# Kernel tuning notes

Measured on AMD Instinct MI355X. Metric: run time of the kernel, lower is better.

Reference implementation:

```python
import jax, jax.numpy as jnp
import numpy as np

N, D, INNER, HIDDEN, CLASSES = 2048, 64, 32, 2048, 10
P = D * (D - 1) // 2  # 2016 pairwise units


def setup_inputs() -> dict:
    key = jax.random.key(0)
    k = jax.random.split(key, 7)
    x = jax.random.normal(k[0], (N, D), dtype=jnp.float32)
    # pairwise Linear(2, inner): stacked weights [P, 2, INNER]
    Wu = jax.random.normal(k[1], (P, 2, INNER), dtype=jnp.float32) * (1.0 / np.sqrt(2.0))
    bu = jax.random.normal(k[2], (P, INNER), dtype=jnp.float32) * 0.01
    Wv = jax.random.normal(k[3], (P * INNER, HIDDEN), dtype=jnp.float32) * (1.0 / np.sqrt(P * INNER))
    bv = jax.random.normal(k[4], (HIDDEN,), dtype=jnp.float32) * 0.01
    Wo = jax.random.normal(k[5], (HIDDEN, CLASSES), dtype=jnp.float32) * (1.0 / np.sqrt(HIDDEN))
    bo = jax.random.normal(k[6], (CLASSES,), dtype=jnp.float32) * 0.01
    return {"x": x, "Wu": Wu, "bu": bu, "Wv": Wv, "bv": bv, "Wo": Wo, "bo": bo}


def reference(x, Wu, bu, Wv, bv, Wo, bo):
    d = x.shape[1]
    ii, jj = np.triu_indices(d, k=1)  # static pair indices, P pairs
    # gather all pairwise 2-vectors in one shot: [N, P, 2]
    pairs = jnp.stack([x[:, ii], x[:, jj]], axis=-1)
    # fused batched tiny matmuls + ReLU: [N, P, INNER]
    u = jax.nn.relu(jnp.einsum('npt,pti->npi', pairs, Wu) + bu)
    u_concat = u.reshape(u.shape[0], -1)  # [N, P*INNER]
    v = jax.nn.relu(u_concat @ Wv + bv)   # [N, HIDDEN]
    return v @ Wo + bo                    # [N, CLASSES]
```

## Files before the change

kernel.cpp:

```cpp
#include <hip/hip_runtime.h>
#include <stdint.h>
#include <stddef.h>

#define N_ 2048
#define D_ 64
#define INNER_ 32
#define HIDDEN_ 2048
#define CLASSES_ 10
#define P_ 2016
#define K_ (P_ * INNER_)
#define SPLITK 4
#define KCHUNK (K_ / SPLITK)
#define BM 128
#define BN 128
#define BK 32
#define TBM 256
#define TBN 256
#define TBK 16
#define NBUF 4

typedef __bf16 bf16x8 __attribute__((ext_vector_type(8)));
typedef __bf16 bf16x4 __attribute__((ext_vector_type(4)));
typedef float f32x16 __attribute__((ext_vector_type(16)));
typedef float f32x4v __attribute__((ext_vector_type(4)));
typedef float f32x2v __attribute__((ext_vector_type(2)));
typedef __attribute__((address_space(1))) void gvoid_t;
typedef __attribute__((address_space(3))) void lvoid_t;

__global__ __launch_bounds__(256) void k_u(const float* __restrict__ x,
                                           const float* __restrict__ Wu,
                                           const float* __restrict__ bu,
                                           __bf16* __restrict__ u) {
  const int t = threadIdx.x;
  const int n0 = blockIdx.y * 4;
  __shared__ float xs[4][D_];
  __shared__ int iis[32], jjs[32];
  xs[t >> 6][t & 63] = x[(size_t)(n0 + (t >> 6)) * D_ + (t & 63)];
  if (t < 32) {
    const int p = blockIdx.x * 32 + t;
    int ii = (int)floorf((127.0f - sqrtf(16129.0f - 8.0f * (float)p)) * 0.5f);
    int off = ii * 63 - (ii * (ii - 1)) / 2;
    while (p >= off + (63 - ii)) { off += 63 - ii; ++ii; }
    while (p < off)              { --ii; off -= 63 - ii; }
    iis[t] = ii;
    jjs[t] = (p - off) + ii + 1;
  }
  __syncthreads();
  const int k0 = blockIdx.x * 1024 + t * 4;
  const int pl = t >> 3;
  const int i0 = (t & 7) * 4;
  const int p  = blockIdx.x * 32 + pl;
  const float4 w0 = *(const float4*)(Wu + (size_t)p * 64 + i0);
  const float4 w1 = *(const float4*)(Wu + (size_t)p * 64 + 32 + i0);
  const float4 bb = *(const float4*)(bu + (size_t)p * 32 + i0);
  const int ii = iis[pl], jj = jjs[pl];
#pragma unroll
  for (int nn = 0; nn < 4; ++nn) {
    const float xi = xs[nn][ii], xj = xs[nn][jj];
    bf16x4 r;
    r[0] = (__bf16)fmaxf(fmaf(xi, w0.x, fmaf(xj, w1.x, bb.x)), 0.0f);
    r[1] = (__bf16)fmaxf(fmaf(xi, w0.y, fmaf(xj, w1.y, bb.y)), 0.0f);
    r[2] = (__bf16)fmaxf(fmaf(xi, w0.z, fmaf(xj, w1.z, bb.z)), 0.0f);
    r[3] = (__bf16)fmaxf(fmaf(xi, w0.w, fmaf(xj, w1.w, bb.w)), 0.0f);
    *(bf16x4*)(u + (size_t)(n0 + nn) * K_ + k0) = r;
  }
}

__global__ __launch_bounds__(256) void k_tr(const float* __restrict__ Wv,
                                            __bf16* __restrict__ BT) {
  __shared__ float ls[64][65];
  const int t = threadIdx.x;
  const int k0 = blockIdx.x * 64, h0 = blockIdx.y * 64;
  const int c4 = (t & 15) * 4, r0 = t >> 4;
#pragma unroll
  for (int s = 0; s < 4; ++s) {
    const int r = r0 + 16 * s;
    const float4 vv = *(const float4*)(Wv + (size_t)(k0 + r) * HIDDEN_ + h0 + c4);
    ls[r][c4] = vv.x; ls[r][c4 + 1] = vv.y; ls[r][c4 + 2] = vv.z; ls[r][c4 + 3] = vv.w;
  }
  __syncthreads();
#pragma unroll
  for (int s = 0; s < 2; ++s) {
    const int item = s * 256 + t;
    const int h = item >> 3;
    const int kch = item & 7;
    bf16x8 o;
#pragma unroll
    for (int j = 0; j < 8; ++j) o[j] = (__bf16)ls[kch * 8 + j][h];
    *(bf16x8*)(BT + (size_t)(h0 + h) * K_ + k0 + kch * 8) = o;
  }
}

__global__ __launch_bounds__(512, 2) void k_gemm3(const __bf16* __restrict__ A,
                                                  const __bf16* __restrict__ BT,
                                                  float* __restrict__ part) {
  __shared__ __align__(16) __bf16 lds[NBUF][2][TBM][TBK];

  const int t = threadIdx.x;
  const int lane = t & 63;
  const int w = t >> 6;
  const int wm = w & 3, wn = w >> 2;
  const int l31 = lane & 31, khalf = lane >> 5;

  const int id = blockIdx.x;
  const int g = id & 7, s = id >> 3;
  const int bm = ((g >> 2) << 2) + (s & 3);
  const int bn = ((g & 3) << 1) + ((s >> 2) & 1);
  const int kc = s >> 3;
  const int mbase = bm * TBM, hbase = bn * TBN;

  const int srow = t >> 1;
  const int sgc = (t & 1) ^ ((srow >> 2) & 1);
  const __bf16* gA = A + (size_t)(mbase + srow) * K_ + (size_t)kc * KCHUNK + sgc * 8;
  const __bf16* gB = BT + (size_t)(hbase + srow) * K_ + (size_t)kc * KCHUNK + sgc * 8;
  const uint32_t lOff = (uint32_t)((t & ~63) * 16);
  char* ldsbase = (char*)&lds[0][0][0][0];

  int aoff[2], boff[4];
#pragma unroll
  for (int mf = 0; mf < 2; ++mf) {
    const int row = wm * 64 + mf * 32 + l31;
    const int cpos = khalf ^ ((row >> 2) & 1);
    aoff[mf] = row * TBK + cpos * 8;
  }
#pragma unroll
  for (int nf = 0; nf < 4; ++nf) {
    const int row = wn * 128 + nf * 32 + l31;
    const int cpos = khalf ^ ((row >> 2) & 1);
    boff[nf] = TBM * TBK + row * TBK + cpos * 8;
  }

  f32x16 acc[2][4] = {};

#define STAGE_TILE(BUF)                                                                        \
  do {                                                                                         \
    char* dst_ = ldsbase + (size_t)(BUF) * 16384;                                              \
    __builtin_amdgcn_global_load_lds((gvoid_t*)(uintptr_t)gA,                                  \
                                     (lvoid_t*)(uint32_t)(uintptr_t)(dst_ + lOff), 16, 0, 0);  \
    __builtin_amdgcn_global_load_lds((gvoid_t*)(uintptr_t)gB,                                  \
                                     (lvoid_t*)(uint32_t)(uintptr_t)(dst_ + 8192 + lOff), 16, 0, 0); \
    gA += TBK;                                                                                 \
    gB += TBK;                                                                                 \
  } while (0)

#define FRAG_READS(T)                                                                          \
  const __bf16* plane = (const __bf16*)(ldsbase + (size_t)((T) & 3) * 16384);                  \
  bf16x8 av[2], bv4[4];                                                                        \
  _Pragma("unroll") for (int mf = 0; mf < 2; ++mf)                                             \
      av[mf] = *(const bf16x8*)(plane + aoff[mf]);                                             \
  _Pragma("unroll") for (int nf = 0; nf < 4; ++nf)                                             \
      bv4[nf] = *(const bf16x8*)(plane + boff[nf]);

#define MFMA_CLUSTER()                                                                         \
  __builtin_amdgcn_s_setprio(1);                                                               \
  _Pragma("unroll") for (int mf = 0; mf < 2; ++mf)                                             \
      _Pragma("unroll") for (int nf = 0; nf < 4; ++nf)                                         \
          acc[mf][nf] = __builtin_amdgcn_mfma_f32_32x32x16_bf16(av[mf], bv4[nf],               \
                                                                acc[mf][nf], 0, 0, 0);         \
  __builtin_amdgcn_s_setprio(0);

  STAGE_TILE(0);
  STAGE_TILE(1);
  STAGE_TILE(2);
  asm volatile("s_waitcnt vmcnt(4)" ::: "memory");
  __builtin_amdgcn_s_barrier();
  __builtin_amdgcn_sched_barrier(0);

  const int ksteps = KCHUNK / TBK;

  for (int t0 = 0; t0 < ksteps - 3; ++t0) {
    FRAG_READS(t0);
    STAGE_TILE((t0 + 3) & 3);
    __builtin_amdgcn_s_barrier();
    MFMA_CLUSTER();
    asm volatile("s_waitcnt vmcnt(4)" ::: "memory");
    __builtin_amdgcn_s_barrier();
    __builtin_amdgcn_sched_barrier(0);
  }
  {
    FRAG_READS(ksteps - 3);
    __builtin_amdgcn_s_barrier();
    MFMA_CLUSTER();
    asm volatile("s_waitcnt vmcnt(2)" ::: "memory");
    __builtin_amdgcn_s_barrier();
    __builtin_amdgcn_sched_barrier(0);
  }
  {
    FRAG_READS(ksteps - 2);
    __builtin_amdgcn_s_barrier();
    MFMA_CLUSTER();
    asm volatile("s_waitcnt vmcnt(0)" ::: "memory");
    __builtin_amdgcn_s_barrier();
    __builtin_amdgcn_sched_barrier(0);
  }
  {
    FRAG_READS(ksteps - 1);
    __builtin_amdgcn_s_barrier();
    MFMA_CLUSTER();
  }
#undef STAGE_TILE
#undef FRAG_READS
#undef MFMA_CLUSTER

  float* op = part + ((size_t)kc * N_ + mbase + wm * 64) * HIDDEN_ + hbase + wn * 128;
#pragma unroll
  for (int mf = 0; mf < 2; ++mf)
#pragma unroll
    for (int nf = 0; nf < 4; ++nf)
#pragma unroll
      for (int rg = 0; rg < 16; ++rg) {
        const int row = mf * 32 + (rg & 3) + 8 * (rg >> 2) + 4 * khalf;
        op[(size_t)row * HIDDEN_ + nf * 32 + l31] = acc[mf][nf][rg];
      }
}

__global__ __launch_bounds__(256) void k_gemm_fb(const __bf16* __restrict__ A,
                                                 const float* __restrict__ Bv,
                                                 float* __restrict__ part) {
  __shared__ __bf16 As[BM][BK];
  __shared__ __bf16 BsT[BN][36];

  const int t = threadIdx.x;
  const int lane = t & 63;
  const int w = t >> 6, wm = w >> 1, wn = w & 1;
  const int l15 = lane & 15, q = lane >> 4;
  const int bn = blockIdx.x, bm = blockIdx.y, kc = blockIdx.z;
  const int mbase = bm * BM, hbase = bn * BN;
  const int n0 = (t & 63) * 2;
  const int kq = t >> 6;
  const int kx = (q ^ ((l15 >> 1) & 3)) * 8;

  const bf16x8* ap[4];
  const bf16x8* bp[4];
#pragma unroll
  for (int mf = 0; mf < 4; ++mf) ap[mf] = (const bf16x8*)&As[wm * 64 + mf * 16 + l15][kx];
#pragma unroll
  for (int nf = 0; nf < 4; ++nf) bp[nf] = (const bf16x8*)&BsT[wn * 64 + nf * 16 + l15][q * 8];

  f32x4v acc[4][4] = {};

  const int ksteps = KCHUNK / BK;
  for (int ks = 0; ks < ksteps; ++ks) {
    const int kbase = kc * KCHUNK + ks * BK;
    const float* gb = Bv + (size_t)(kbase + kq * 8) * HIDDEN_ + hbase + n0;
    f32x2v f[8];
#pragma unroll
    for (int qq = 0; qq < 8; ++qq) f[qq] = *(const f32x2v*)(gb + (size_t)qq * HIDDEN_);

    __syncthreads();
#pragma unroll
    for (int r = 0; r < 2; ++r) {
      const int flat = r * 256 + t;
      const int row = flat >> 2;
      const int gc = (flat & 3) ^ ((row >> 1) & 3);
      const __bf16* ga = A + (size_t)(mbase + row) * K_ + kbase + gc * 8;
      void* lp = (char*)&As[0][0] + (size_t)(r * 256 + (t & ~63)) * 16;
      __builtin_amdgcn_global_load_lds((gvoid_t*)(uintptr_t)ga,
                                       (lvoid_t*)(uint32_t)(uintptr_t)lp, 16, 0, 0);
    }
    bf16x8 c0, c1;
#pragma unroll
    for (int qq = 0; qq < 8; ++qq) { c0[qq] = (__bf16)f[qq][0]; c1[qq] = (__bf16)f[qq][1]; }
    *(bf16x8*)&BsT[n0][kq * 8]     = c0;
    *(bf16x8*)&BsT[n0 + 1][kq * 8] = c1;

    __syncthreads();

    bf16x8 av[4], bv4[4];
#pragma unroll
    for (int mf = 0; mf < 4; ++mf) av[mf] = *ap[mf];
#pragma unroll
    for (int nf = 0; nf < 4; ++nf) bv4[nf] = *bp[nf];
#pragma unroll
    for (int mf = 0; mf < 4; ++mf)
#pragma unroll
      for (int nf = 0; nf < 4; ++nf)
        acc[mf][nf] = __builtin_amdgcn_mfma_f32_16x16x32_bf16(av[mf], bv4[nf], acc[mf][nf], 0, 0, 0);
  }

  float* op = part + ((size_t)kc * N_ + mbase + wm * 64) * HIDDEN_ + hbase + wn * 64;
#pragma unroll
  for (int mf = 0; mf < 4; ++mf)
#pragma unroll
    for (int nf = 0; nf < 4; ++nf)
#pragma unroll
      for (int r = 0; r < 4; ++r)
        op[(size_t)(mf * 16 + q * 4 + r) * HIDDEN_ + nf * 16 + l15] = acc[mf][nf][r];
}

__global__ __launch_bounds__(256) void k_reduce(const float* __restrict__ part,
                                                const float* __restrict__ bv,
                                                float* __restrict__ v) {
  const size_t i = ((size_t)blockIdx.x * 256 + threadIdx.x) * 4;
  f32x4v s = *(const f32x4v*)(part + i);
  s += *(const f32x4v*)(part + (size_t)1 * N_ * HIDDEN_ + i);
  s += *(const f32x4v*)(part + (size_t)2 * N_ * HIDDEN_ + i);
  s += *(const f32x4v*)(part + (size_t)3 * N_ * HIDDEN_ + i);
  s += *(const f32x4v*)(bv + (i & (HIDDEN_ - 1)));
  s[0] = fmaxf(s[0], 0.0f);
  s[1] = fmaxf(s[1], 0.0f);
  s[2] = fmaxf(s[2], 0.0f);
  s[3] = fmaxf(s[3], 0.0f);
  *(f32x4v*)(v + i) = s;
}

__global__ __launch_bounds__(256) void k_out(const float* __restrict__ v,
                                             const float* __restrict__ Wo,
                                             const float* __restrict__ bo,
                                             float* __restrict__ out) {
  const int lane = threadIdx.x & 63;
  const int n = blockIdx.x * 4 + (threadIdx.x >> 6);
  float acc[CLASSES_];
#pragma unroll
  for (int c = 0; c < CLASSES_; ++c) acc[c] = 0.0f;
  for (int h0 = lane * 4; h0 < HIDDEN_; h0 += 256) {
    const f32x4v vv = *(const f32x4v*)(v + (size_t)n * HIDDEN_ + h0);
#pragma unroll
    for (int qq = 0; qq < 4; ++qq) {
      const float s = vv[qq];
      const float* wo = Wo + (size_t)(h0 + qq) * CLASSES_;
#pragma unroll
      for (int c = 0; c < CLASSES_; ++c) acc[c] = fmaf(s, wo[c], acc[c]);
    }
  }
#pragma unroll
  for (int c = 0; c < CLASSES_; ++c) {
#pragma unroll
    for (int o = 32; o > 0; o >>= 1) acc[c] += __shfl_down(acc[c], o);
  }
  if (lane == 0) {
#pragma unroll
    for (int c = 0; c < CLASSES_; ++c) out[(size_t)n * CLASSES_ + c] = acc[c] + bo[c];
  }
}

extern "C" void kernel_launch(void* const* d_in, const int* in_sizes, int n_in,
                              void* d_out, int out_size, void* d_ws, size_t ws_size,
                              hipStream_t stream) {
  const float* x  = (const float*)d_in[0];
  const float* Wu = (const float*)d_in[1];
  const float* bu = (const float*)d_in[2];
  const float* Wv = (const float*)d_in[3];
  const float* bv = (const float*)d_in[4];
  const float* Wo = (const float*)d_in[5];
  const float* bo = (const float*)d_in[6];
  float* out = (float*)d_out;

  char* ws = (char*)d_ws;
  const size_t SZ_BT = (size_t)HIDDEN_ * K_ * 2;
  const size_t SZ_U  = (size_t)N_ * K_ * 2;
  const size_t SZ_P  = (size_t)SPLITK * N_ * HIDDEN_ * 4;
  const size_t NEED  = SZ_BT + SZ_U + SZ_P;

  if (ws_size >= NEED) {
    __bf16* BT  = (__bf16*)ws;
    __bf16* u   = (__bf16*)(ws + SZ_BT);
    float* part = (float*)(ws + SZ_BT + SZ_U);
    float* v    = (float*)ws;

    k_u<<<dim3(K_ / 1024, N_ / 4), 256, 0, stream>>>(x, Wu, bu, u);
    k_tr<<<dim3(K_ / 64, HIDDEN_ / 64), 256, 0, stream>>>(Wv, BT);
    k_gemm3<<<dim3((HIDDEN_ / TBN) * (N_ / TBM) * SPLITK), 512, 0, stream>>>(u, BT, part);
    k_reduce<<<dim3((N_ * HIDDEN_) / 1024), 256, 0, stream>>>(part, bv, v);
    k_out<<<dim3(N_ / 4), 256, 0, stream>>>(v, Wo, bo, out);
  } else {
    __bf16* u   = (__bf16*)ws;
    float* part = (float*)(ws + SZ_U);
    float* v    = (float*)(ws + SZ_U + SZ_P);

    k_u<<<dim3(K_ / 1024, N_ / 4), 256, 0, stream>>>(x, Wu, bu, u);
    k_gemm_fb<<<dim3(HIDDEN_ / BN, N_ / BM, SPLITK), 256, 0, stream>>>(u, Wv, part);
    k_reduce<<<dim3((N_ * HIDDEN_) / 1024), 256, 0, stream>>>(part, bv, v);
    k_out<<<dim3(N_ / 4), 256, 0, stream>>>(v, Wo, bo, out);
  }
}
```

Before: 1.405 ms.

## Deepen LDS ring to eight stages and double-buffer fragment registers

```diff
diff --git a/kernel.cpp b/kernel.cpp
--- a/kernel.cpp
+++ b/kernel.cpp
@@ -17,7 +17,7 @@
 #define TBM 256
 #define TBN 256
 #define TBK 16
-#define NBUF 4
+#define NBUF 8
 
 typedef __bf16 bf16x8 __attribute__((ext_vector_type(8)));
 typedef __bf16 bf16x4 __attribute__((ext_vector_type(4)));
@@ -131,6 +131,9 @@
   }
 
   f32x16 acc[2][4] = {};
+  bf16x8 avA[2], bvA[4], avB[2], bvB[4];
+
+#define VMCNT(N) asm volatile("s_waitcnt vmcnt(" #N ")" ::: "memory")
 
 #define STAGE_TILE(BUF)                                                                        \
   do {                                                                                         \
@@ -143,64 +146,71 @@
     gB += TBK;                                                                                 \
   } while (0)
 
-#define FRAG_READS(T)                                                                          \
-  const __bf16* plane = (const __bf16*)(ldsbase + (size_t)((T) & 3) * 16384);                  \
-  bf16x8 av[2], bv4[4];                                                                        \
-  _Pragma("unroll") for (int mf = 0; mf < 2; ++mf)                                             \
-      av[mf] = *(const bf16x8*)(plane + aoff[mf]);                                             \
-  _Pragma("unroll") for (int nf = 0; nf < 4; ++nf)                                             \
-      bv4[nf] = *(const bf16x8*)(plane + boff[nf]);
-
-#define MFMA_CLUSTER()                                                                         \
-  __builtin_amdgcn_s_setprio(1);                                                               \
-  _Pragma("unroll") for (int mf = 0; mf < 2; ++mf)                                             \
-      _Pragma("unroll") for (int nf = 0; nf < 4; ++nf)                                         \
-          acc[mf][nf] = __builtin_amdgcn_mfma_f32_32x32x16_bf16(av[mf], bv4[nf],               \
-                                                                acc[mf][nf], 0, 0, 0);         \
-  __builtin_amdgcn_s_setprio(0);
+#define FRAG_READ_TO(T, AV, BV)                                                                \
+  do {                                                                                         \
+    const __bf16* plane_ = (const __bf16*)(ldsbase + (size_t)((T) & 7) * 16384);               \
+    _Pragma("unroll") for (int mf = 0; mf < 2; ++mf)                                           \
+        AV[mf] = *(const bf16x8*)(plane_ + aoff[mf]);                                          \
+    _Pragma("unroll") for (int nf = 0; nf < 4; ++nf)                                           \
+        BV[nf] = *(const bf16x8*)(plane_ + boff[nf]);                                          \
+  } while (0)
+
+#define MFMA_ON(AV, BV)                                                                        \
+  do {                                                                                         \
+    __builtin_amdgcn_s_setprio(1);                                                             \
+    _Pragma("unroll") for (int mf = 0; mf < 2; ++mf)                                           \
+        _Pragma("unroll") for (int nf = 0; nf < 4; ++nf)                                       \
+            acc[mf][nf] = __builtin_amdgcn_mfma_f32_32x32x16_bf16(AV[mf], BV[nf],              \
+                                                                  acc[mf][nf], 0, 0, 0);       \
+    __builtin_amdgcn_s_setprio(0);                                                             \
+  } while (0)
+
+#define BODY(T, AVc, BVc, AVn, BVn, DOSTAGE, GATE)                                             \
+  do {                                                                                         \
+    if (DOSTAGE) STAGE_TILE(((T) + 7) & 7);                                                    \
+    FRAG_READ_TO((T) + 1, AVn, BVn);                                                           \
+    __builtin_amdgcn_sched_barrier(0);                                                         \
+    MFMA_ON(AVc, BVc);                                                                         \
+    VMCNT(GATE);                                                                               \
+    __builtin_amdgcn_s_barrier();                                                              \
+    __builtin_amdgcn_sched_barrier(0);                                                         \
+  } while (0)
 
   STAGE_TILE(0);
   STAGE_TILE(1);
   STAGE_TILE(2);
-  asm volatile("s_waitcnt vmcnt(4)" ::: "memory");
+  STAGE_TILE(3);
+  STAGE_TILE(4);
+  STAGE_TILE(5);
+  STAGE_TILE(6);
+  VMCNT(10);
   __builtin_amdgcn_s_barrier();
   __builtin_amdgcn_sched_barrier(0);
 
   const int ksteps = KCHUNK / TBK;
 
-  for (int t0 = 0; t0 < ksteps - 3; ++t0) {
-    FRAG_READS(t0);
-    STAGE_TILE((t0 + 3) & 3);
-    __builtin_amdgcn_s_barrier();
-    MFMA_CLUSTER();
-    asm volatile("s_waitcnt vmcnt(4)" ::: "memory");
-    __builtin_amdgcn_s_barrier();
-    __builtin_amdgcn_sched_barrier(0);
-  }
-  {
-    FRAG_READS(ksteps - 3);
-    __builtin_amdgcn_s_barrier();
-    MFMA_CLUSTER();
-    asm volatile("s_waitcnt vmcnt(2)" ::: "memory");
-    __builtin_amdgcn_s_barrier();
-    __builtin_amdgcn_sched_barrier(0);
-  }
-  {
-    FRAG_READS(ksteps - 2);
-    __builtin_amdgcn_s_barrier();
-    MFMA_CLUSTER();
-    asm volatile("s_waitcnt vmcnt(0)" ::: "memory");
-    __builtin_amdgcn_s_barrier();
-    __builtin_amdgcn_sched_barrier(0);
-  }
-  {
-    FRAG_READS(ksteps - 1);
-    __builtin_amdgcn_s_barrier();
-    MFMA_CLUSTER();
-  }
+  FRAG_READ_TO(0, avA, bvA);
+
+  BODY(0, avA, bvA, avB, bvB, 1, 10);
+  for (int t0 = 1; t0 + 1 <= ksteps - 8; t0 += 2) {
+    BODY(t0, avB, bvB, avA, bvA, 1, 10);
+    BODY(t0 + 1, avA, bvA, avB, bvB, 1, 10);
+  }
+  BODY(ksteps - 7, avB, bvB, avA, bvA, 0, 8);
+  BODY(ksteps - 6, avA, bvA, avB, bvB, 0, 6);
+  BODY(ksteps - 5, avB, bvB, avA, bvA, 0, 4);
+  BODY(ksteps - 4, avA, bvA, avB, bvB, 0, 2);
+  BODY(ksteps - 3, avB, bvB, avA, bvA, 0, 0);
+  FRAG_READ_TO(ksteps - 1, avB, bvB);
+  __builtin_amdgcn_sched_barrier(0);
+  MFMA_ON(avA, bvA);
+  MFMA_ON(avB, bvB);
+
+#undef BODY
+#undef MFMA_ON
+#undef FRAG_READ_TO
 #undef STAGE_TILE
-#undef FRAG_READS
-#undef MFMA_CLUSTER
+#undef VMCNT
 
   float* op = part + ((size_t)kc * N_ + mbase + wm * 64) * HIDDEN_ + hbase + wn * 128;
 #pragma unroll
```

Measured after the change: 1.419 ms. About the same (+1.0%).
